# Kernel tuning notes

Measured on AMD Instinct MI355X. Metric: run time of the kernel, lower is better.

The kernel has to match this reference:

```python
import jax, jax.numpy as jnp
import numpy as np

N = 16384          # replayed items
D_STATE = 2048     # state_dim
D_SEM = 1024       # semantic_dim
S = 4096           # num_semantic_slots
LR = 0.01
DIST_THRESH = 2.0


def setup_inputs() -> dict:
    key = jax.random.key(0)
    k1, k2, k3 = jax.random.split(key, 3)
    replayed_states = jax.random.normal(k1, (N, D_STATE), dtype=jnp.float32)
    replayed_rewards = jax.random.normal(k2, (N,), dtype=jnp.float32)
    # small weight scale so projected content std ~0.05 -> nearest distances
    # straddle the 2.0 threshold and both branches get exercised
    W = jax.random.normal(k3, (D_SEM, D_STATE), dtype=jnp.float32) * (0.05 / np.sqrt(D_STATE))
    b = jnp.zeros((D_SEM,), dtype=jnp.float32)
    semantic_traces = jnp.zeros((S, D_SEM), dtype=jnp.float32)
    trace_strengths = jnp.zeros((S,), dtype=jnp.float32)
    return {
        "replayed_states": replayed_states,
        "replayed_rewards": replayed_rewards,
        "W": W,
        "b": b,
        "semantic_traces": semantic_traces,
        "trace_strengths": trace_strengths,
    }


def _consolidate(content_all, rewards, traces0, strengths0):
    slot_ids = jnp.arange(S, dtype=jnp.int32)

    def step(carry, xs):
        traces, strengths, ptr, num = carry
        content, reward = xs
        reward = jnp.abs(reward)
        valid = jnp.minimum(num, S)
        # euclidean distances to valid slots (invalid -> +inf)
        d = jnp.sqrt(jnp.sum((traces - content[None, :]) ** 2, axis=1))
        d = jnp.where(slot_ids < valid, d, jnp.inf)
        nearest = jnp.argmin(d).astype(jnp.int32)
        nearest_dist = d[nearest]
        do_update = (num > 0) & (nearest_dist < DIST_THRESH)

        # branch A: EMA update of nearest slot
        eff_lr = LR * (1.0 + reward)
        delta = content - traces[nearest]
        traces_u = traces.at[nearest].add(delta * eff_lr)
        strengths_u = strengths.at[nearest].add(1.0)

        # branch B: insert at ring-buffer ptr
        traces_i = traces.at[ptr].set(content)
        strengths_i = strengths.at[ptr].set(1.0)
        ptr_i = (ptr + 1) % S
        num_i = jnp.minimum(num + 1, S)

        traces_n = jnp.where(do_update, traces_u, traces_i)
        strengths_n = jnp.where(do_update, strengths_u, strengths_i)
        ptr_n = jnp.where(do_update, ptr, ptr_i)
        num_n = jnp.where(do_update, num, num_i)
        return (traces_n, strengths_n, ptr_n, num_n), None

    init = (traces0, strengths0, jnp.int32(0), jnp.int32(0))
    (traces, strengths, ptr, num), _ = jax.lax.scan(step, init, (content_all, rewards))
    return traces, strengths, num


def reference(replayed_states, replayed_rewards, W, b, semantic_traces, trace_strengths):
    # projection: nn.Linear -> x @ W.T + b
    content_all = replayed_states @ W.T + b  # (N, D_SEM)
    traces, strengths, num = _consolidate(
        content_all, replayed_rewards, semantic_traces, trace_strengths
    )
    valid_mask = (jnp.arange(S) < jnp.minimum(num, S)).astype(jnp.float32)
    denom = jnp.maximum(valid_mask.sum(), 1.0)
    mean_strength = jnp.where(num > 0, (strengths * valid_mask).sum() / denom, 0.0)
    num_consolidated = jnp.int32(N)  # every item either updates or inserts
    return traces, strengths, num, num_consolidated, mean_strength


if __name__ == "__main__":
    out = reference(**setup_inputs())
    print([getattr(o, "shape", o) for o in out])
```

## Files before the change

kernel.cpp:

```cpp
#include <hip/hip_runtime.h>
#include <cstdint>
#include <cstddef>

#define N_ITEMS 16384
#define D_STATE 2048
#define D_SEM   1024
#define S_SLOTS 4096
#define DTHRESH 2.0f

#define B_ITEMS 256
#define NBLK    (N_ITEMS / B_ITEMS)
#define CHUNK_BLKS 16
#define CHUNK_ITEMS (B_ITEMS * CHUNK_BLKS)

typedef unsigned long long u64;
typedef unsigned int u32;

__global__ __launch_bounds__(256)
void gemm_kernel(const float* __restrict__ A, const float* __restrict__ W,
                 const float* __restrict__ bias, float* __restrict__ C) {
  __shared__ float As[16][68];
  __shared__ float Bs[16][68];
  const int t = threadIdx.x;
  const int ty = t >> 4, tx = t & 15;
  const int i0 = blockIdx.x * 64, j0 = blockIdx.y * 64;
  const int lrow = t >> 2, lcol = (t & 3) << 2;
  float acc[4][4] = {{0.f}};
  const float* ap = A + (size_t)(i0 + lrow) * D_STATE + lcol;
  const float* wp = W + (size_t)(j0 + lrow) * D_STATE + lcol;
  for (int k0 = 0; k0 < D_STATE; k0 += 16) {
    float4 av = *(const float4*)(ap + k0);
    float4 wv = *(const float4*)(wp + k0);
    __syncthreads();
    As[lcol + 0][lrow] = av.x; As[lcol + 1][lrow] = av.y;
    As[lcol + 2][lrow] = av.z; As[lcol + 3][lrow] = av.w;
    Bs[lcol + 0][lrow] = wv.x; Bs[lcol + 1][lrow] = wv.y;
    Bs[lcol + 2][lrow] = wv.z; Bs[lcol + 3][lrow] = wv.w;
    __syncthreads();
#pragma unroll
    for (int kk = 0; kk < 16; kk++) {
      float a[4], b[4];
#pragma unroll
      for (int y = 0; y < 4; y++) a[y] = As[kk][ty * 4 + y];
#pragma unroll
      for (int x = 0; x < 4; x++) b[x] = Bs[kk][tx * 4 + x];
#pragma unroll
      for (int y = 0; y < 4; y++)
#pragma unroll
        for (int x = 0; x < 4; x++) acc[y][x] = fmaf(a[y], b[x], acc[y][x]);
    }
  }
#pragma unroll
  for (int y = 0; y < 4; y++)
#pragma unroll
    for (int x = 0; x < 4; x++) {
      const int col = j0 + tx * 4 + x;
      C[(size_t)(i0 + ty * 4 + y) * D_SEM + col] = acc[y][x] + bias[col];
    }
}

__global__ __launch_bounds__(256)
void gram_kernel(const float* __restrict__ Cc, float* __restrict__ G) {
  const int z = blockIdx.z;
  const float* A = Cc + (size_t)z * B_ITEMS * D_SEM;
  __shared__ float As[16][68];
  __shared__ float Bs[16][68];
  const int t = threadIdx.x;
  const int ty = t >> 4, tx = t & 15;
  const int i0 = blockIdx.x * 64, j0 = blockIdx.y * 64;
  const int lrow = t >> 2, lcol = (t & 3) << 2;
  float acc[4][4] = {{0.f}};
  const float* ap = A + (size_t)(i0 + lrow) * D_SEM + lcol;
  const float* wp = A + (size_t)(j0 + lrow) * D_SEM + lcol;
  for (int k0 = 0; k0 < D_SEM; k0 += 16) {
    float4 av = *(const float4*)(ap + k0);
    float4 wv = *(const float4*)(wp + k0);
    __syncthreads();
    As[lcol + 0][lrow] = av.x; As[lcol + 1][lrow] = av.y;
    As[lcol + 2][lrow] = av.z; As[lcol + 3][lrow] = av.w;
    Bs[lcol + 0][lrow] = wv.x; Bs[lcol + 1][lrow] = wv.y;
    Bs[lcol + 2][lrow] = wv.z; Bs[lcol + 3][lrow] = wv.w;
    __syncthreads();
#pragma unroll
    for (int kk = 0; kk < 16; kk++) {
      float a[4], b[4];
#pragma unroll
      for (int y = 0; y < 4; y++) a[y] = As[kk][ty * 4 + y];
#pragma unroll
      for (int x = 0; x < 4; x++) b[x] = Bs[kk][tx * 4 + x];
#pragma unroll
      for (int y = 0; y < 4; y++)
#pragma unroll
        for (int x = 0; x < 4; x++) acc[y][x] = fmaf(a[y], b[x], acc[y][x]);
    }
  }
  float* Gz = G + (size_t)z * B_ITEMS * B_ITEMS;
#pragma unroll
  for (int y = 0; y < 4; y++)
#pragma unroll
    for (int x = 0; x < 4; x++)
      Gz[(size_t)(i0 + ty * 4 + y) * B_ITEMS + j0 + tx * 4 + x] = acc[y][x];
}

__global__ __launch_bounds__(256)
void pgemm_kernel(const float* __restrict__ A,
                  const float* __restrict__ T,
                  float* __restrict__ P,
                  const int* __restrict__ state) {
  const int limit = min(state[0] + B_ITEMS, S_SLOTS);
  const int j0 = blockIdx.y * 64;
  const int i0 = blockIdx.x * 64;
  const int t = threadIdx.x;
  const int ty = t >> 4, tx = t & 15;
  if (j0 >= limit) {
    const float4 z = {0.f, 0.f, 0.f, 0.f};
    const int col = j0 + tx * 4;
#pragma unroll
    for (int y = 0; y < 4; y++)
      *(float4*)(P + (size_t)(i0 + ty * 4 + y) * S_SLOTS + col) = z;
    return;
  }
  __shared__ float As[16][68];
  __shared__ float Bs[16][68];
  const int lrow = t >> 2, lcol = (t & 3) << 2;
  float acc[4][4] = {{0.f}};
  const float* ap = A + (size_t)(i0 + lrow) * D_SEM + lcol;
  const float* wp = T + (size_t)(j0 + lrow) * D_SEM + lcol;
  for (int k0 = 0; k0 < D_SEM; k0 += 16) {
    float4 av = *(const float4*)(ap + k0);
    float4 wv = *(const float4*)(wp + k0);
    __syncthreads();
    As[lcol + 0][lrow] = av.x; As[lcol + 1][lrow] = av.y;
    As[lcol + 2][lrow] = av.z; As[lcol + 3][lrow] = av.w;
    Bs[lcol + 0][lrow] = wv.x; Bs[lcol + 1][lrow] = wv.y;
    Bs[lcol + 2][lrow] = wv.z; Bs[lcol + 3][lrow] = wv.w;
    __syncthreads();
#pragma unroll
    for (int kk = 0; kk < 16; kk++) {
      float a[4], b[4];
#pragma unroll
      for (int y = 0; y < 4; y++) a[y] = As[kk][ty * 4 + y];
#pragma unroll
      for (int x = 0; x < 4; x++) b[x] = Bs[kk][tx * 4 + x];
#pragma unroll
      for (int y = 0; y < 4; y++)
#pragma unroll
        for (int x = 0; x < 4; x++) acc[y][x] = fmaf(a[y], b[x], acc[y][x]);
    }
  }
#pragma unroll
  for (int y = 0; y < 4; y++)
#pragma unroll
    for (int x = 0; x < 4; x++)
      P[(size_t)(i0 + ty * 4 + y) * S_SLOTS + j0 + tx * 4 + x] = acc[y][x];
}

__global__ __launch_bounds__(256)
void init_kernel(const float* __restrict__ traces0, float* __restrict__ out,
                 float* __restrict__ n_g, int* __restrict__ state) {
  __shared__ float wsum[4];
  const int s = blockIdx.x, t = threadIdx.x;
  const int lane = t & 63, wave = t >> 6;
  float4 v = *(const float4*)(traces0 + (size_t)s * D_SEM + 4 * t);
  *(float4*)(out + (size_t)s * D_SEM + 4 * t) = v;
  float nn = v.x * v.x + v.y * v.y + v.z * v.z + v.w * v.w;
#pragma unroll
  for (int o = 32; o; o >>= 1) nn += __shfl_down(nn, o, 64);
  if (lane == 0) wsum[wave] = nn;
  __syncthreads();
  if (t == 0) n_g[s] = wsum[0] + wsum[1] + wsum[2] + wsum[3];
  if (s == 0 && t == 0) { state[0] = 0; state[1] = 0; }
}

__global__ __launch_bounds__(256, 1)
void scan_kernel(const float* __restrict__ P, const float* __restrict__ Gb,
                 const float* __restrict__ rewards, const float* __restrict__ n_g,
                 int* __restrict__ state, u64* __restrict__ decs) {
  __shared__ float corr_buf[S_SLOTS];
  __shared__ u64 partials[4];
  const int t = threadIdx.x;
  const int lane = t & 63, wave = t >> 6;
  const int s_base = t << 4;

  int num = state[0];
  int ptr = state[1];

  for (int s = t; s < S_SLOTS; s += 256) corr_buf[s] = 0.f;

  float n_reg[16];
#pragma unroll
  for (int k = 0; k < 16; k += 4) {
    float4 nv = *(const float4*)(n_g + s_base + k);
    n_reg[k + 0] = (s_base + k + 0 < num) ? nv.x : __uint_as_float(0x7F800000u);
    n_reg[k + 1] = (s_base + k + 1 < num) ? nv.y : __uint_as_float(0x7F800000u);
    n_reg[k + 2] = (s_base + k + 2 < num) ? nv.z : __uint_as_float(0x7F800000u);
    n_reg[k + 3] = (s_base + k + 3 < num) ? nv.w : __uint_as_float(0x7F800000u);
  }
  float alpha_r[16];
#pragma unroll
  for (int k = 0; k < 16; k++) alpha_r[k] = 1.f;

  float p_cur[16], p_n1[16], p_in[16];
#pragma unroll
  for (int k = 0; k < 16; k += 4) {
    float4 v0 = *(const float4*)(P + s_base + k);
    float4 v1 = *(const float4*)(P + (size_t)S_SLOTS + s_base + k);
    p_cur[k] = v0.x; p_cur[k + 1] = v0.y; p_cur[k + 2] = v0.z; p_cur[k + 3] = v0.w;
    p_n1[k]  = v1.x; p_n1[k + 1]  = v1.y; p_n1[k + 2]  = v1.z; p_n1[k + 3]  = v1.w;
  }
#pragma unroll
  for (int k = 0; k < 16; k++) p_in[k] = 0.f;

  float p_raw_a[16], p_raw_b[16];
  float gc_a, gc_b;
  {
    const float* rp = P + (size_t)2 * S_SLOTS + s_base;
#pragma unroll
    for (int k = 0; k < 16; k += 4) {
      float4 v = *(const float4*)(rp + k);
      p_raw_a[k] = v.x; p_raw_a[k + 1] = v.y; p_raw_a[k + 2] = v.z; p_raw_a[k + 3] = v.w;
    }
    gc_a = Gb[(size_t)2 * B_ITEMS + t];
    gc_b = 0.f;
#pragma unroll
    for (int k = 0; k < 16; k++) p_raw_b[k] = 0.f;
  }

  float gi = Gb[0];
  float ri = rewards[0];
  float g1 = Gb[1];

  int my_cslot = -1; float my_coeff = 0.f;
  u32 my_slot = 0; float my_lr = 0.f;

  __syncthreads();

#define OWNFIX(K, I) { const float nold = n_reg[K]; \
    if (upd) { const float pc = 0.5f * (nold + gi - d2b); \
      n_reg[K] = omr * omr * nold + 2.0f * lr * omr * pc + lr * lr * gi; \
      alpha_r[K] = __fmul_rn(alpha_r[K], omr); \
      if ((I) + 1 < B_ITEMS) p_n1[K] = fmaf(omr, p_n1[K], __fmul_rn(lr, g1)); \
    } else { n_reg[K] = gi; alpha_r[K] = 0.f; \
      if ((I) + 1 < B_ITEMS) p_n1[K] = g1; } }

#define SCAN_STEP(I, RAWC, GCC, RAWN, GCN) { \
     \
    if ((I) + 3 < B_ITEMS) { \
      const float* rp = P + (size_t)((I) + 3) * S_SLOTS + s_base; \
      _Pragma("unroll") \
      for (int k = 0; k < 16; k += 4) { \
        float4 v = *(const float4*)(rp + k); \
        RAWN[k] = v.x; RAWN[k + 1] = v.y; RAWN[k + 2] = v.z; RAWN[k + 3] = v.w; \
      } \
      GCN = Gb[(size_t)((I) + 3) * B_ITEMS + t]; \
    } \
    float gi_n = 0.f, ri_n = 0.f, g1_n = 0.f; \
    if ((I) + 1 < B_ITEMS) { \
      gi_n = Gb[(size_t)((I) + 1) * B_ITEMS + (I) + 1]; \
      ri_n = rewards[(I) + 1]; \
      if ((I) + 2 < B_ITEMS) g1_n = Gb[(size_t)((I) + 1) * B_ITEMS + (I) + 2]; \
    } \
     \
    u64 best = ~0ull; \
    _Pragma("unroll") \
    for (int k = 0; k < 16; k++) { \
      const float d2 = fmaxf(fmaf(-2.0f, p_cur[k], n_reg[k] + gi), 0.f); \
      const u64 key = ((u64)__float_as_uint(d2) << 32) | (u32)(s_base + k); \
      if (key < best) best = key; \
    } \
    _Pragma("unroll") \
    for (int o = 32; o; o >>= 1) { \
      const u64 v = __shfl_down(best, o, 64); \
      if (v < best) best = v; \
    } \
    if (lane == 0) partials[wave] = best; \
    asm volatile("s_waitcnt lgkmcnt(0)" ::: "memory"); \
    __builtin_amdgcn_s_barrier(); \
    __builtin_amdgcn_sched_barrier(0); \
     \
    u64 bk = partials[0]; \
    { u64 v = partials[1]; if (v < bk) bk = v; \
      v = partials[2]; if (v < bk) bk = v; \
      v = partials[3]; if (v < bk) bk = v; } \
    const float d2b = __uint_as_float((u32)(bk >> 32)); \
    const int nslot = (int)(u32)bk; \
    const bool upd = (num > 0) && (d2b < 4.0f); \
    const float lr = __fmul_rn(0.01f, __fadd_rn(1.0f, fabsf(ri))); \
    const int slot = upd ? nslot : ptr; \
    const float omr = 1.0f - lr; \
    if (!upd) { num = min(num + 1, S_SLOTS); ptr = (ptr + 1) & (S_SLOTS - 1); } \
    if ((I) == t) { my_slot = (u32)slot | (upd ? 0x80000000u : 0u); my_lr = lr; } \
    if (my_cslot == slot) my_coeff = upd ? __fmul_rn(my_coeff, omr) : 0.f; \
    if ((I) == t) { my_cslot = slot; my_coeff = upd ? lr : 1.f; } \
    if ((slot >> 4) == t) { \
      switch (slot & 15) { \
        case 0:  OWNFIX(0,  I) break; case 1:  OWNFIX(1,  I) break; \
        case 2:  OWNFIX(2,  I) break; case 3:  OWNFIX(3,  I) break; \
        case 4:  OWNFIX(4,  I) break; case 5:  OWNFIX(5,  I) break; \
        case 6:  OWNFIX(6,  I) break; case 7:  OWNFIX(7,  I) break; \
        case 8:  OWNFIX(8,  I) break; case 9:  OWNFIX(9,  I) break; \
        case 10: OWNFIX(10, I) break; case 11: OWNFIX(11, I) break; \
        case 12: OWNFIX(12, I) break; case 13: OWNFIX(13, I) break; \
        case 14: OWNFIX(14, I) break; default: OWNFIX(15, I) break; \
      } \
    } \
     \
    if ((I) + 2 < B_ITEMS && my_coeff != 0.f) \
      atomicAdd(&corr_buf[my_cslot], __fmul_rn(my_coeff, GCC)); \
    asm volatile("s_waitcnt lgkmcnt(0)" ::: "memory"); \
    __builtin_amdgcn_s_barrier(); \
    __builtin_amdgcn_sched_barrier(0); \
     \
    if ((I) + 2 < B_ITEMS) { \
      const float4 z4 = {0.f, 0.f, 0.f, 0.f}; \
      _Pragma("unroll") \
      for (int k = 0; k < 16; k += 4) { \
        float4 cv = *(const float4*)(&corr_buf[s_base + k]); \
        p_in[k + 0] = fmaf(alpha_r[k + 0], RAWC[k + 0], cv.x); \
        p_in[k + 1] = fmaf(alpha_r[k + 1], RAWC[k + 1], cv.y); \
        p_in[k + 2] = fmaf(alpha_r[k + 2], RAWC[k + 2], cv.z); \
        p_in[k + 3] = fmaf(alpha_r[k + 3], RAWC[k + 3], cv.w); \
        *(float4*)(&corr_buf[s_base + k]) = z4; \
      } \
    } \
     \
    _Pragma("unroll") \
    for (int k = 0; k < 16; k++) { p_cur[k] = p_n1[k]; p_n1[k] = p_in[k]; } \
    gi = gi_n; ri = ri_n; g1 = g1_n; \
  }

  for (int i = 0; i < B_ITEMS; i += 2) {
    SCAN_STEP(i,     p_raw_a, gc_a, p_raw_b, gc_b)
    SCAN_STEP(i + 1, p_raw_b, gc_b, p_raw_a, gc_a)
  }
#undef SCAN_STEP
#undef OWNFIX

  if (t == 0) { state[0] = num; state[1] = ptr; }
  decs[t] = ((u64)__float_as_uint(my_lr) << 32) | (u64)my_slot;
}

__global__ __launch_bounds__(256)
void apply_kernel(const float* __restrict__ content,
                  const u64* __restrict__ decs,
                  float* __restrict__ traces,
                  float* __restrict__ n_g) {
  __shared__ u32 aslot[B_ITEMS];
  __shared__ float alr[B_ITEMS];
  __shared__ float betas[B_ITEMS];
  __shared__ int notowner;
  __shared__ float wsum[4];
  const int t = threadIdx.x, j = blockIdx.x;
  const int lane = t & 63, wave = t >> 6;
  const u64 d = decs[t];
  aslot[t] = (u32)(d & 0xFFFFFFFFull);
  alr[t] = __uint_as_float((u32)(d >> 32));
  if (t == 0) notowner = 0;
  __syncthreads();
  const u32 myslot = aslot[j] & 0x7FFFFFFFu;
  if (t > j && (aslot[t] & 0x7FFFFFFFu) == myslot) notowner = 1;
  __syncthreads();
  if (notowner) return;

  float alpha = 1.f, beta = 0.f;
  for (int k = 0; k < B_ITEMS; k++) {
    const u32 a = aslot[k];
    if ((a & 0x7FFFFFFFu) == myslot) {
      const float lr = alr[k];
      if (a & 0x80000000u) {
        const float om = 1.f - lr;
        alpha *= om; beta *= om;
        if (t == k) beta += lr;
      } else {
        alpha = 0.f; beta = (t == k) ? 1.f : 0.f;
      }
    }
  }
  betas[t] = beta;
  __syncthreads();

  float4 v = *(const float4*)(traces + (size_t)myslot * D_SEM + 4 * t);
  v.x *= alpha; v.y *= alpha; v.z *= alpha; v.w *= alpha;
  for (int k = 0; k < B_ITEMS; k++) {
    if ((aslot[k] & 0x7FFFFFFFu) == myslot) {
      const float bk = betas[k];
      const float4 c = *(const float4*)(content + (size_t)k * D_SEM + 4 * t);
      v.x = fmaf(bk, c.x, v.x); v.y = fmaf(bk, c.y, v.y);
      v.z = fmaf(bk, c.z, v.z); v.w = fmaf(bk, c.w, v.w);
    }
  }
  *(float4*)(traces + (size_t)myslot * D_SEM + 4 * t) = v;
  float nn = v.x * v.x + v.y * v.y + v.z * v.z + v.w * v.w;
#pragma unroll
  for (int o = 32; o; o >>= 1) nn += __shfl_down(nn, o, 64);
  if (lane == 0) wsum[wave] = nn;
  __syncthreads();
  if (t == 0) n_g[myslot] = wsum[0] + wsum[1] + wsum[2] + wsum[3];
}

__global__ __launch_bounds__(256)
void finalize_kernel(const float* __restrict__ strengths0,
                     const u64* __restrict__ decs,
                     const int* __restrict__ state, float* __restrict__ out) {
  __shared__ int last_ins[S_SLOTS];
  __shared__ int cnt[S_SLOTS];
  __shared__ float wsum[4];
  const int t = threadIdx.x, lane = t & 63, wave = t >> 6;
  for (int s = t; s < S_SLOTS; s += 256) { last_ins[s] = -1; cnt[s] = 0; }
  __syncthreads();
  for (int k = t; k < N_ITEMS; k += 256) {
    const u32 dd = (u32)(decs[k] & 0xFFFFFFFFull);
    if (!(dd & 0x80000000u)) atomicMax(&last_ins[(int)dd], k);
  }
  __syncthreads();
  for (int k = t; k < N_ITEMS; k += 256) {
    const u32 dd = (u32)(decs[k] & 0xFFFFFFFFull);
    const int slot = (int)(dd & 0x7FFFFFFFu);
    if ((dd & 0x80000000u) && k > last_ins[slot]) atomicAdd(&cnt[slot], 1);
  }
  __syncthreads();
  const int num = state[0];
  float* outs = out + (size_t)S_SLOTS * D_SEM;
  float lsum = 0.f;
  for (int s = t; s < S_SLOTS; s += 256) {
    const float base = (last_ins[s] >= 0) ? 1.f : strengths0[s];
    const float v = base + (float)cnt[s];
    outs[s] = v;
    if (s < num) lsum += v;
  }
#pragma unroll
  for (int o = 32; o; o >>= 1) lsum += __shfl_down(lsum, o, 64);
  if (lane == 0) wsum[wave] = lsum;
  __syncthreads();
  if (t == 0) {
    const float total = wsum[0] + wsum[1] + wsum[2] + wsum[3];
    float denom = (float)num;
    if (denom < 1.f) denom = 1.f;
    outs[S_SLOTS + 0] = (float)num;
    outs[S_SLOTS + 1] = (float)N_ITEMS;
    outs[S_SLOTS + 2] = (num > 0) ? (total / denom) : 0.f;
  }
}

extern "C" void kernel_launch(void* const* d_in, const int* in_sizes, int n_in,
                              void* d_out, int out_size, void* d_ws, size_t ws_size,
                              hipStream_t stream) {
  const float* states  = (const float*)d_in[0];
  const float* rewards = (const float*)d_in[1];
  const float* W       = (const float*)d_in[2];
  const float* bias    = (const float*)d_in[3];
  const float* traces0 = (const float*)d_in[4];
  const float* str0    = (const float*)d_in[5];
  float* out = (float*)d_out;

  char* p = (char*)d_ws;
  float* cbuf = (float*)p;                 p += (size_t)CHUNK_ITEMS * D_SEM * 4;
  float* P    = (float*)p;                 p += (size_t)B_ITEMS * S_SLOTS * 4;
  float* Gb   = (float*)p;                 p += (size_t)CHUNK_BLKS * B_ITEMS * B_ITEMS * 4;
  float* n_g  = (float*)p;                 p += (size_t)S_SLOTS * 4;
  u64*   decs = (u64*)p;                   p += (size_t)N_ITEMS * 8;
  int*   state = (int*)p;

  init_kernel<<<S_SLOTS, 256, 0, stream>>>(traces0, out, n_g, state);

  for (int c = 0; c < N_ITEMS / CHUNK_ITEMS; c++) {
    gemm_kernel<<<dim3(CHUNK_ITEMS / 64, D_SEM / 64), 256, 0, stream>>>(
        states + (size_t)c * CHUNK_ITEMS * D_STATE, W, bias, cbuf);
    gram_kernel<<<dim3(4, 4, CHUNK_BLKS), 256, 0, stream>>>(cbuf, Gb);
    for (int bb = 0; bb < CHUNK_BLKS; bb++) {
      const int b = c * CHUNK_BLKS + bb;
      const float* cblk = cbuf + (size_t)bb * B_ITEMS * D_SEM;
      const float* Gblk = Gb + (size_t)bb * B_ITEMS * B_ITEMS;
      pgemm_kernel<<<dim3(4, S_SLOTS / 64), 256, 0, stream>>>(cblk, out, P, state);
      scan_kernel<<<1, 256, 0, stream>>>(P, Gblk, rewards + (size_t)b * B_ITEMS,
                                         n_g, state, decs + (size_t)b * B_ITEMS);
      apply_kernel<<<B_ITEMS, 256, 0, stream>>>(cblk, decs + (size_t)b * B_ITEMS,
                                                out, n_g);
    }
  }
  finalize_kernel<<<1, 256, 0, stream>>>(str0, decs, state, out);
}
```

Before: 35.84 ms.

## Halve scan-step barriers with double-buffered correction buffers and DPP wave argmin

The sequential scan kernel now double-buffers the shared correction buffer and the partials array, which removes the second block barrier in each scan step. The atomic correction adds move before the argmin, and the owner fixup patches the loaded correction values directly so the step stays consistent. The wave argmin now does an in-register tree over 16 keys, a DPP float min, and a ballot/readlane, replacing 64-bit shuffles. A padded, swizzled LDS layout is meant to avoid bank conflicts. The cost is more LDS, extra register pressure, and subtle ordering correctness risk.

```diff
diff --git a/kernel.cpp b/kernel.cpp
--- a/kernel.cpp
+++ b/kernel.cpp
@@ -172,20 +172,42 @@
   if (s == 0 && t == 0) { state[0] = 0; state[1] = 0; }
 }
 
+__device__ __forceinline__ float wave_min_f32(float x) {
+  int xi = __float_as_int(x), y;
+  y = __builtin_amdgcn_update_dpp(xi, xi, 0x111, 0xF, 0xF, false);
+  x = fminf(x, __int_as_float(y)); xi = __float_as_int(x);
+  y = __builtin_amdgcn_update_dpp(xi, xi, 0x112, 0xF, 0xF, false);
+  x = fminf(x, __int_as_float(y)); xi = __float_as_int(x);
+  y = __builtin_amdgcn_update_dpp(xi, xi, 0x114, 0xF, 0xF, false);
+  x = fminf(x, __int_as_float(y)); xi = __float_as_int(x);
+  y = __builtin_amdgcn_update_dpp(xi, xi, 0x118, 0xF, 0xF, false);
+  x = fminf(x, __int_as_float(y)); xi = __float_as_int(x);
+  y = __builtin_amdgcn_update_dpp(xi, xi, 0x142, 0xA, 0xF, false);
+  x = fminf(x, __int_as_float(y)); xi = __float_as_int(x);
+  y = __builtin_amdgcn_update_dpp(xi, xi, 0x143, 0xC, 0xF, false);
+  x = fminf(x, __int_as_float(y)); xi = __float_as_int(x);
+  return __int_as_float(__builtin_amdgcn_readlane(xi, 63));
+}
+
+#define CORR_SZ 4352
+#define SWZ(s) ((s) + ((s) >> 4))
+
 __global__ __launch_bounds__(256, 1)
 void scan_kernel(const float* __restrict__ P, const float* __restrict__ Gb,
                  const float* __restrict__ rewards, const float* __restrict__ n_g,
                  int* __restrict__ state, u64* __restrict__ decs) {
-  __shared__ float corr_buf[S_SLOTS];
-  __shared__ u64 partials[4];
+  __shared__ float corr0[CORR_SZ];
+  __shared__ float corr1[CORR_SZ];
+  __shared__ u64 partials[2][4];
   const int t = threadIdx.x;
   const int lane = t & 63, wave = t >> 6;
   const int s_base = t << 4;
+  const int c_base = 17 * t;
 
   int num = state[0];
   int ptr = state[1];
 
-  for (int s = t; s < S_SLOTS; s += 256) corr_buf[s] = 0.f;
+  for (int s = t; s < CORR_SZ; s += 256) { corr0[s] = 0.f; corr1[s] = 0.f; }
 
   float n_reg[16];
 #pragma unroll
@@ -200,7 +222,7 @@
 #pragma unroll
   for (int k = 0; k < 16; k++) alpha_r[k] = 1.f;
 
-  float p_cur[16], p_n1[16], p_in[16];
+  float p_cur[16], p_n1[16];
 #pragma unroll
   for (int k = 0; k < 16; k += 4) {
     float4 v0 = *(const float4*)(P + s_base + k);
@@ -208,8 +230,6 @@
     p_cur[k] = v0.x; p_cur[k + 1] = v0.y; p_cur[k + 2] = v0.z; p_cur[k + 3] = v0.w;
     p_n1[k]  = v1.x; p_n1[k + 1]  = v1.y; p_n1[k + 2]  = v1.z; p_n1[k + 3]  = v1.w;
   }
-#pragma unroll
-  for (int k = 0; k < 16; k++) p_in[k] = 0.f;
 
   float p_raw_a[16], p_raw_b[16];
   float gc_a, gc_b;
@@ -240,10 +260,12 @@
       n_reg[K] = omr * omr * nold + 2.0f * lr * omr * pc + lr * lr * gi; \
       alpha_r[K] = __fmul_rn(alpha_r[K], omr); \
       if ((I) + 1 < B_ITEMS) p_n1[K] = fmaf(omr, p_n1[K], __fmul_rn(lr, g1)); \
+      if ((I) + 2 < B_ITEMS) cv[K] = fmaf(omr, cv[K], __fmul_rn(lr, gf)); \
     } else { n_reg[K] = gi; alpha_r[K] = 0.f; \
-      if ((I) + 1 < B_ITEMS) p_n1[K] = g1; } }
-
-#define SCAN_STEP(I, RAWC, GCC, RAWN, GCN) { \
+      if ((I) + 1 < B_ITEMS) p_n1[K] = g1; \
+      if ((I) + 2 < B_ITEMS) cv[K] = gf; } }
+
+#define SCAN_STEP(I, CBUF, RAWC, GCC, RAWN, GCN) { \
      \
     if ((I) + 3 < B_ITEMS) { \
       const float* rp = P + (size_t)((I) + 3) * S_SLOTS + s_base; \
@@ -254,34 +276,54 @@
       } \
       GCN = Gb[(size_t)((I) + 3) * B_ITEMS + t]; \
     } \
-    float gi_n = 0.f, ri_n = 0.f, g1_n = 0.f; \
+    float gi_n = 0.f, ri_n = 0.f, g1_n = 0.f, gf = 0.f; \
     if ((I) + 1 < B_ITEMS) { \
       gi_n = Gb[(size_t)((I) + 1) * B_ITEMS + (I) + 1]; \
       ri_n = rewards[(I) + 1]; \
       if ((I) + 2 < B_ITEMS) g1_n = Gb[(size_t)((I) + 1) * B_ITEMS + (I) + 2]; \
     } \
-     \
-    u64 best = ~0ull; \
+    if ((I) + 2 < B_ITEMS) gf = Gb[(size_t)(I) * B_ITEMS + (I) + 2]; \
+     \
+    if ((I) + 2 < B_ITEMS && my_coeff != 0.f) \
+      atomicAdd(&CBUF[SWZ(my_cslot)], __fmul_rn(my_coeff, GCC)); \
+     \
+    u64 kk[16]; \
     _Pragma("unroll") \
     for (int k = 0; k < 16; k++) { \
-      const float d2 = fmaxf(fmaf(-2.0f, p_cur[k], n_reg[k] + gi), 0.f); \
-      const u64 key = ((u64)__float_as_uint(d2) << 32) | (u32)(s_base + k); \
-      if (key < best) best = key; \
+      const float v = fmaf(-2.0f, p_cur[k], n_reg[k] + gi); \
+      const float d2 = (v > 0.f) ? v : 0.f; \
+      kk[k] = ((u64)__float_as_uint(d2) << 32) | (u32)(s_base + k); \
     } \
     _Pragma("unroll") \
-    for (int o = 32; o; o >>= 1) { \
-      const u64 v = __shfl_down(best, o, 64); \
-      if (v < best) best = v; \
-    } \
-    if (lane == 0) partials[wave] = best; \
+    for (int st = 1; st < 16; st <<= 1) \
+      _Pragma("unroll") \
+      for (int k = 0; k < 16; k += 2 * st) \
+        if (kk[k + st] < kk[k]) kk[k] = kk[k + st]; \
+    const float d2loc = __uint_as_float((u32)(kk[0] >> 32)); \
+    const u32 sloc = (u32)kk[0]; \
+     \
+    const float dmin = wave_min_f32(d2loc); \
+    const u64 bmask = __ballot(d2loc == dmin); \
+    const int bl = __ffsll((unsigned long long)bmask) - 1; \
+    const u32 swave = (u32)__builtin_amdgcn_readlane((int)sloc, bl); \
+    if (lane == 0) \
+      partials[(I) & 1][wave] = ((u64)__float_as_uint(dmin) << 32) | swave; \
     asm volatile("s_waitcnt lgkmcnt(0)" ::: "memory"); \
     __builtin_amdgcn_s_barrier(); \
     __builtin_amdgcn_sched_barrier(0); \
      \
-    u64 bk = partials[0]; \
-    { u64 v = partials[1]; if (v < bk) bk = v; \
-      v = partials[2]; if (v < bk) bk = v; \
-      v = partials[3]; if (v < bk) bk = v; } \
+    u64 bk = partials[(I) & 1][0]; \
+    { u64 v = partials[(I) & 1][1]; if (v < bk) bk = v; \
+      v = partials[(I) & 1][2]; if (v < bk) bk = v; \
+      v = partials[(I) & 1][3]; if (v < bk) bk = v; } \
+    float cv[16]; \
+    if ((I) + 2 < B_ITEMS) { \
+      _Pragma("unroll") \
+      for (int k = 0; k < 16; k++) cv[k] = CBUF[c_base + k]; \
+    } else { \
+      _Pragma("unroll") \
+      for (int k = 0; k < 16; k++) cv[k] = 0.f; \
+    } \
     const float d2b = __uint_as_float((u32)(bk >> 32)); \
     const int nslot = (int)(u32)bk; \
     const bool upd = (num > 0) && (d2b < 4.0f); \
@@ -292,6 +334,7 @@
     if ((I) == t) { my_slot = (u32)slot | (upd ? 0x80000000u : 0u); my_lr = lr; } \
     if (my_cslot == slot) my_coeff = upd ? __fmul_rn(my_coeff, omr) : 0.f; \
     if ((I) == t) { my_cslot = slot; my_coeff = upd ? lr : 1.f; } \
+     \
     if ((slot >> 4) == t) { \
       switch (slot & 15) { \
         case 0:  OWNFIX(0,  I) break; case 1:  OWNFIX(1,  I) break; \
@@ -305,33 +348,21 @@
       } \
     } \
      \
-    if ((I) + 2 < B_ITEMS && my_coeff != 0.f) \
-      atomicAdd(&corr_buf[my_cslot], __fmul_rn(my_coeff, GCC)); \
-    asm volatile("s_waitcnt lgkmcnt(0)" ::: "memory"); \
-    __builtin_amdgcn_s_barrier(); \
-    __builtin_amdgcn_sched_barrier(0); \
-     \
+    _Pragma("unroll") \
+    for (int k = 0; k < 16; k++) p_cur[k] = p_n1[k]; \
     if ((I) + 2 < B_ITEMS) { \
-      const float4 z4 = {0.f, 0.f, 0.f, 0.f}; \
       _Pragma("unroll") \
-      for (int k = 0; k < 16; k += 4) { \
-        float4 cv = *(const float4*)(&corr_buf[s_base + k]); \
-        p_in[k + 0] = fmaf(alpha_r[k + 0], RAWC[k + 0], cv.x); \
-        p_in[k + 1] = fmaf(alpha_r[k + 1], RAWC[k + 1], cv.y); \
-        p_in[k + 2] = fmaf(alpha_r[k + 2], RAWC[k + 2], cv.z); \
-        p_in[k + 3] = fmaf(alpha_r[k + 3], RAWC[k + 3], cv.w); \
-        *(float4*)(&corr_buf[s_base + k]) = z4; \
+      for (int k = 0; k < 16; k++) { \
+        p_n1[k] = fmaf(alpha_r[k], RAWC[k], cv[k]); \
+        CBUF[c_base + k] = 0.f; \
       } \
     } \
-     \
-    _Pragma("unroll") \
-    for (int k = 0; k < 16; k++) { p_cur[k] = p_n1[k]; p_n1[k] = p_in[k]; } \
     gi = gi_n; ri = ri_n; g1 = g1_n; \
   }
 
   for (int i = 0; i < B_ITEMS; i += 2) {
-    SCAN_STEP(i,     p_raw_a, gc_a, p_raw_b, gc_b)
-    SCAN_STEP(i + 1, p_raw_b, gc_b, p_raw_a, gc_a)
+    SCAN_STEP(i,     corr0, p_raw_a, gc_a, p_raw_b, gc_b)
+    SCAN_STEP(i + 1, corr1, p_raw_b, gc_b, p_raw_a, gc_a)
   }
 #undef SCAN_STEP
 #undef OWNFIX
```

After: 32.26 ms. -10.0%, faster.
